# Kernel optimization log

Measured on AMD Instinct MI355X. Metric: run time of the kernel, lower is better.

The kernel has to match this reference:

```python
import jax, jax.numpy as jnp
import numpy as np

B, S, N = 4, 512, 2048
E = 1024          # expanded_size
QL, H, D, VL = 32, 8, 2, 32   # query_len, num_heads, num_duplicates, values_len
EPS = 1e-5


def setup_inputs() -> dict:
    key = jax.random.key(0)
    ks = jax.random.split(key, 8)
    return {
        "embeddings": jax.random.normal(ks[0], (B, S, E), jnp.float32),
        "keys": jax.random.normal(ks[1], (B, N, QL * H), jnp.float32),
        "values": jax.random.normal(ks[2], (B, N, VL * H), jnp.float32),
        "output_connectivity_sub": jax.random.normal(ks[3], (H, S * D, N), jnp.float32),
        "Wq": jax.random.normal(ks[4], (QL * H * D, E), jnp.float32) / np.sqrt(E),
        "bq": jnp.zeros((QL * H * D,), jnp.float32),
        "Wo": jax.random.normal(ks[5], (E, VL * H * D), jnp.float32) / np.sqrt(VL * H * D),
        "bo": jnp.zeros((E,), jnp.float32),
        "gamma": jnp.ones((VL * H * D,), jnp.float32),
        "beta": jnp.zeros((VL * H * D,), jnp.float32),
    }


def reference(embeddings, keys, values, output_connectivity_sub,
              Wq, bq, Wo, bo, gamma, beta):
    # query projection: [B,S,E] -> [B,S,QL*H*D]
    q = embeddings @ Wq.T + bq
    # view [B, S*D, QL*H] -> [B, S*D, QL, H] -> [B, H, S*D, QL]
    q = q.reshape(B, S * D, QL, H).transpose(0, 3, 1, 2)
    # keys: [B,N,QL*H] -> [B,N,QL,H] -> [B,H,QL,N]
    k = keys.reshape(B, N, QL, H).transpose(0, 3, 2, 1)
    # values: [B,N,VL*H] -> [B,N,VL,H] -> [B,H,N,VL]
    v = values.reshape(B, N, VL, H).transpose(0, 3, 1, 2)

    scores = jnp.einsum('bhsq,bhqn->bhsn', q, k) / np.sqrt(QL).astype(np.float32)
    probs = jax.nn.softmax(scores - output_connectivity_sub, axis=-1)
    vo = jnp.einsum('bhsn,bhnv->bhsv', probs, v)          # [B,H,S*D,VL]

    # [B,H,S*D,VL] -> [B,H,S,VL*D] -> [B,S,H,VL*D] -> [B,S,H*VL*D]
    vo = vo.reshape(B, H, S, VL * D).transpose(0, 2, 1, 3).reshape(B, S, H * VL * D)

    mean = jnp.mean(vo, axis=-1, keepdims=True)
    var = jnp.mean(jnp.square(vo - mean), axis=-1, keepdims=True)
    xn = (vo - mean) / jnp.sqrt(var + EPS) * gamma + beta
    return xn @ Wo.T + bo
```

## Files before the change

kernel.cpp:

```cpp
#include <hip/hip_runtime.h>
#include <hip/hip_bf16.h>


typedef short  short8 __attribute__((ext_vector_type(8)));
typedef float  f32x4  __attribute__((ext_vector_type(4)));

__device__ __forceinline__ ushort f2bf(float x) {
  union { float f; unsigned int u; } v; v.f = x;
  unsigned int r = v.u + 0x7fffu + ((v.u >> 16) & 1u);
  return (ushort)(r >> 16);
}

__device__ __forceinline__ unsigned int cvtpk(float a, float b) {
  unsigned int r;
  asm("v_cvt_pk_bf16_f32 %0, %1, %2" : "=v"(r) : "v"(a), "v"(b));
  return r;
}
__device__ __forceinline__ short8 cvt8(f32x4 a, f32x4 b) {
  union { unsigned int u[4]; short8 s; } r;
  r.u[0] = cvtpk(a[0], a[1]);
  r.u[1] = cvtpk(a[2], a[3]);
  r.u[2] = cvtpk(b[0], b[1]);
  r.u[3] = cvtpk(b[2], b[3]);
  return r.s;
}

#if __has_builtin(__builtin_amdgcn_global_load_lds)
#define OCS_ASYNC 1
__device__ __forceinline__ void gl_lds16(const float* g, float* l) {
  __builtin_amdgcn_global_load_lds(
      (const __attribute__((address_space(1))) unsigned int*)g,
      (__attribute__((address_space(3))) unsigned int*)l, 16, 0, 0);
}
#else
#define OCS_ASYNC 0
#endif

__device__ __forceinline__ void prep_body(
    char* smem, int bi,
    const float* __restrict__ keys, const float* __restrict__ values,
    ushort* __restrict__ kbf, ushort* __restrict__ vbf)
{
  ushort (*T)[264] = (ushort (*)[264])smem;
  const int b  = bi >> 6;
  const int n0 = (bi & 63) * 32;
  const int t  = threadIdx.x;
  const int nr = t >> 3;
  const int c0 = (t & 7) * 32;

  {
    const float* src = keys + ((size_t)b*2048 + n0 + nr)*256 + c0;
#pragma unroll
    for (int j = 0; j < 32; j += 8) {
      f32x4 x0 = *(const f32x4*)(src + j);
      f32x4 x1 = *(const f32x4*)(src + j + 4);
      *(short8*)&T[nr][c0 + j] = cvt8(x0, x1);
    }
  }
  __syncthreads();
  {
    const int h = t >> 5, nn = t & 31;
    const int pp = 16*((nn >> 2) & 1) + 4*(nn >> 3) + (nn & 3);
    ushort* dst = kbf + (((size_t)(b*8 + h) * 2048) + n0 + pp) * 32;
#pragma unroll
    for (int j = 0; j < 4; j++) {
      short8 w;
#pragma unroll
      for (int i = 0; i < 8; i++) w[i] = (short)T[nn][(j*8 + i)*8 + h];
      *(short8*)(dst + j*8) = w;
    }
  }
  __syncthreads();
  {
    const float* src = values + ((size_t)b*2048 + n0 + nr)*256 + c0;
#pragma unroll
    for (int j = 0; j < 32; j += 8) {
      f32x4 x0 = *(const f32x4*)(src + j);
      f32x4 x1 = *(const f32x4*)(src + j + 4);
      *(short8*)&T[nr][c0 + j] = cvt8(x0, x1);
    }
  }
  __syncthreads();
  {
    const int c = t, h = c & 7, vl = c >> 3;
    ushort* dst = vbf + (((size_t)(b*8 + h) * 32) + vl) * 2048 + n0;
#pragma unroll
    for (int j = 0; j < 4; j++) {
      short8 w;
#pragma unroll
      for (int i = 0; i < 8; i++) w[i] = (short)T[j*8 + i][c];
      *(short8*)(dst + j*8) = w;
    }
  }
}

template<int EPI>
__device__ __forceinline__ void gemm_body(
    char* smem,
    const float* __restrict__ A, const float* __restrict__ Bm,
    const float* __restrict__ bias, void* __restrict__ outp,
    int M, int N, int K, int m0, int n0,
    const float* __restrict__ rowsum, const float* __restrict__ rowsumsq,
    const float* __restrict__ gamma,  const float* __restrict__ beta)
{
  ushort* As = (ushort*)smem;
  ushort* Bs = (ushort*)(smem + 8192);
  const int tid = threadIdx.x;
  const int lane = tid & 63;
  const int wid  = tid >> 6;
  const int wm = wid >> 1, wn = wid & 1;
  const int lt = lane & 15, g = lane >> 4;
  const int lrow = tid >> 2;
  const int lseg = tid & 3;
  const int slot_w = lseg ^ ((lrow & 3) ^ ((lrow >> 2) & 3));

  f32x4 acc[2][2] = {};
  f32x4 pa0, pa1, pb0, pb1;

  float mean_r = 0.f, rstd_r = 1.f;
  if (EPI == 1) {
    const float s_  = rowsum[m0 + lrow];
    const float sq_ = rowsumsq[m0 + lrow];
    mean_r = s_ * (1.0f/512.0f);
    rstd_r = rsqrtf(sq_ * (1.0f/512.0f) - mean_r * mean_r + 1e-5f);
  }

#define GLOAD(K0) do {                                                        \
    const float* sa_ = A  + (size_t)(m0 + lrow) * K + (K0) + lseg * 8;        \
    pa0 = *(const f32x4*)sa_;  pa1 = *(const f32x4*)(sa_ + 4);                \
    const float* sb_ = Bm + (size_t)(n0 + lrow) * K + (K0) + lseg * 8;        \
    pb0 = *(const f32x4*)sb_;  pb1 = *(const f32x4*)(sb_ + 4);                \
  } while (0)
#define SWRITE(BUF, K0) do {                                                  \
    f32x4 qa0 = pa0, qa1 = pa1;                                               \
    if (EPI == 1) {                                                           \
      const float* gp_ = gamma + (K0) + lseg * 8;                             \
      const float* bp_ = beta  + (K0) + lseg * 8;                             \
      f32x4 g0_ = *(const f32x4*)gp_, g1_ = *(const f32x4*)(gp_ + 4);         \
      f32x4 b0_ = *(const f32x4*)bp_, b1_ = *(const f32x4*)(bp_ + 4);         \
      _Pragma("unroll")                                                       \
      for (int r_ = 0; r_ < 4; r_++) {                                        \
        qa0[r_] = (qa0[r_] - mean_r) * rstd_r * g0_[r_] + b0_[r_];            \
        qa1[r_] = (qa1[r_] - mean_r) * rstd_r * g1_[r_] + b1_[r_];            \
      }                                                                       \
    }                                                                         \
    *(short8*)&As[(BUF)*2048 + lrow*32 + slot_w * 8] = cvt8(qa0, qa1);        \
    *(short8*)&Bs[(BUF)*2048 + lrow*32 + slot_w * 8] = cvt8(pb0, pb1);        \
  } while (0)

  GLOAD(0);
  SWRITE(0, 0);
  __syncthreads();

  int cur = 0;
  for (int k0 = 0; k0 < K; k0 += 32) {
    const bool more = (k0 + 32 < K);
    if (more) GLOAD(k0 + 32);
    short8 af[2], bfr[2];
#pragma unroll
    for (int ss = 0; ss < 2; ss++) {
      const int ra = wm*32 + ss*16 + lt;
      af[ss]  = *(const short8*)&As[cur*2048 + ra*32 + (g ^ ((ra & 3) ^ ((ra >> 2) & 3))) * 8];
      const int rb = wn*32 + ss*16 + lt;
      bfr[ss] = *(const short8*)&Bs[cur*2048 + rb*32 + (g ^ ((rb & 3) ^ ((rb >> 2) & 3))) * 8];
    }
#pragma unroll
    for (int i = 0; i < 2; i++)
#pragma unroll
      for (int j = 0; j < 2; j++)
        acc[i][j] = __builtin_amdgcn_mfma_f32_16x16x32_bf16(af[i], bfr[j], acc[i][j], 0, 0, 0);
    asm volatile("s_barrier" ::: "memory");
    if (more) {
      SWRITE(cur ^ 1, k0 + 32);
      asm volatile("s_waitcnt lgkmcnt(0)" ::: "memory");
    }
    asm volatile("s_barrier" ::: "memory");
    cur ^= 1;
  }

#pragma unroll
  for (int i = 0; i < 2; i++)
#pragma unroll
    for (int j = 0; j < 2; j++) {
      const int n  = n0 + wn*32 + j*16 + lt;
      const float bv = bias[n];
      const int mb = m0 + wm*32 + i*16 + g*4;
#pragma unroll
      for (int r = 0; r < 4; r++) {
        const int mm = mb + r;
        if (EPI == 0) {
          const float val = (acc[i][j][r] + bv) * 0.17677669529663687f;
          const int bb = mm >> 9, s = mm & 511;
          const int d = n >> 8, ql = (n >> 3) & 31, hh = n & 7;
          const int tt = s*2 + d;
          ((ushort*)outp)[((size_t)(bb*8 + hh) * 1024 + tt) * 32 + ql] = f2bf(val);
        } else {
          ((float*)outp)[(size_t)mm * N + n] = acc[i][j][r] + bv;
        }
      }
    }
#undef GLOAD
#undef SWRITE
}

__global__ __launch_bounds__(256) void prep_gemm0(
    const float* __restrict__ keys, const float* __restrict__ values,
    ushort* __restrict__ kbf, ushort* __restrict__ vbf,
    const float* __restrict__ emb, const float* __restrict__ Wq,
    const float* __restrict__ bq, ushort* __restrict__ qbf)
{
  __shared__ __align__(16) char smem[17408];
  const int bi = blockIdx.x;
  if (bi < 256) {
    prep_body(smem, bi, keys, values, kbf, vbf);
  } else {
    const int gblk = bi - 256;
    const int m0 = (gblk & 31) * 64;
    const int n0 = (gblk >> 5) * 64;
    gemm_body<0>(smem, emb, Wq, bq, (void*)qbf, 2048, 512, 1024, m0, n0,
                 nullptr, nullptr, nullptr, nullptr);
  }
}

__global__ __launch_bounds__(256) void gemm1_ln(
    const float* __restrict__ vo, const float* __restrict__ Wo,
    const float* __restrict__ bo, float* __restrict__ outp,
    const float* __restrict__ rowsum, const float* __restrict__ rowsumsq,
    const float* __restrict__ gamma, const float* __restrict__ beta)
{
  __shared__ __align__(16) char smem[16384];
  gemm_body<1>(smem, vo, Wo, bo, (void*)outp, 2048, 1024, 512,
               blockIdx.x * 64, blockIdx.y * 64, rowsum, rowsumsq, gamma, beta);
}

__global__ __launch_bounds__(256) void attn_kernel(
    const ushort* __restrict__ qbf, const ushort* __restrict__ kbf,
    const ushort* __restrict__ vbf, const float* __restrict__ ocs,
    float* __restrict__ pacc, float* __restrict__ pl, int nsteps)
{
#if OCS_ASYNC
  __shared__ float obuf[4][2048];
#endif
  const int tid  = threadIdx.x;
  const int lane = tid & 63;
  const int id = blockIdx.x;
  const int h   = id & 7;
  const int ttp = (id >> 3) & 15;
  const int c   = id >> 7;
  const int b  = tid >> 6;
  const int wid0 = ((h << 5) + 2*ttp) * 4 + b;
  const int t0 = ttp * 64;
  const int lt = lane & 15, g = lane >> 4;
  const int n_start = c * nsteps * 32;

  const ushort* qp = qbf + (size_t)(b*8 + h) * (1024*32);
  const ushort* kp = kbf + (size_t)(b*8 + h) * (2048*32);
  const ushort* vp = vbf + (size_t)(b*8 + h) * (32*2048);
  const float*  op = ocs + (size_t)h * (1024*2048);

#define NSX(I) (((I) < nsteps) ? (n_start + (I)*32) : n_start)

  const int srow = tid >> 3;
  const int scol = 4 * ((tid & 7) ^ (srow & 7));
  const float* sb0 = op + (size_t)(t0 + srow) * 2048 + scol;
  const float* sb1 = op + (size_t)(t0 + 32 + srow) * 2048 + scol;
#if OCS_ASYNC
  const int ldsw = (tid & 192) * 16;
#define SL_ISSUE(STEP) do {                                                   \
    gl_lds16(sb0 + NSX(STEP), (float*)((char*)obuf + (((STEP) & 3) << 13) + ldsw));        \
    gl_lds16(sb1 + NSX(STEP), (float*)((char*)obuf + (((STEP) & 3) << 13) + 4096 + ldsw)); \
  } while (0)
  const int ro0 = lt * 128;
  const int ro1 = (16 + lt) * 128;
  const int c0x = ((2*g)     ^ (lt & 7)) * 16;
  const int c1x = ((2*g + 1) ^ (lt & 7)) * 16;
#define CO_READ(DST, TILE, STEP) do {                                         \
    const char* bb_ = (const char*)obuf + (((STEP) & 3) << 13) + ((TILE) << 12); \
    DST[0][0] = *(const f32x4*)(bb_ + ro0 + c0x);                             \
    DST[1][0] = *(const f32x4*)(bb_ + ro0 + c1x);                             \
    DST[0][1] = *(const f32x4*)(bb_ + ro1 + c0x);                             \
    DST[1][1] = *(const f32x4*)(bb_ + ro1 + c1x);                             \
  } while (0)
#define PAIR_SYNC() do {                                                      \
    __builtin_amdgcn_sched_barrier(0);                                        \
    asm volatile("s_waitcnt vmcnt(8)" ::: "memory");                          \
    __builtin_amdgcn_sched_barrier(0);                                        \
    __builtin_amdgcn_s_barrier();                                             \
  } while (0)
#else
#define SL_ISSUE(STEP)
#define CO_READ(DST, TILE, STEP) do {                                         \
    const int nn_ = NSX(STEP);                                                \
    const float* r0_ = op + (size_t)(t0 + (TILE)*32 + lt) * 2048 + nn_;       \
    const float* r1_ = op + (size_t)(t0 + (TILE)*32 + 16 + lt) * 2048 + nn_;  \
    DST[0][0] = *(const f32x4*)(r0_ + 8*g);                                   \
    DST[1][0] = *(const f32x4*)(r0_ + 8*g + 4);                               \
    DST[0][1] = *(const f32x4*)(r1_ + 8*g);                                   \
    DST[1][1] = *(const f32x4*)(r1_ + 8*g + 4);                               \
  } while (0)
#define PAIR_SYNC()
#endif

#define LD_KV(KD, VD, NN) do {                                                \
    KD[0] = *(const short8*)(kp + (size_t)((NN) + lt) * 32 + g*8);            \
    KD[1] = *(const short8*)(kp + (size_t)((NN) + 16 + lt) * 32 + g*8);       \
    VD[0] = *(const short8*)(vp + (size_t)lt * 2048 + (NN) + g*8);            \
    VD[1] = *(const short8*)(vp + (size_t)(16 + lt) * 2048 + (NN) + g*8);     \
  } while (0)

  short8 qf0[2], qf1[2];
#pragma unroll
  for (int ts = 0; ts < 2; ts++) {
    qf0[ts] = *(const short8*)(qp + (t0 + ts*16 + lt)*32 + g*8);
    qf1[ts] = *(const short8*)(qp + (t0 + 32 + ts*16 + lt)*32 + g*8);
  }

  f32x4 acc0[2][2] = {}, acc1[2][2] = {};
  float lsum0[2] = {0.f, 0.f}, lsum1[2] = {0.f, 0.f};
  const f32x4 fzero = {0.f, 0.f, 0.f, 0.f};

#define TSB(SC0, SC1, CO0, CO1, VLO, VHI, LS, ACCA, ACCB) do {                \
    float p0 = __expf(SC0[0] - CO0[0]);                                       \
    float p1 = __expf(SC0[1] - CO0[1]);                                       \
    float p2 = __expf(SC0[2] - CO0[2]);                                       \
    float p3 = __expf(SC0[3] - CO0[3]);                                       \
    float p4 = __expf(SC1[0] - CO1[0]);                                       \
    float p5 = __expf(SC1[1] - CO1[1]);                                       \
    float p6 = __expf(SC1[2] - CO1[2]);                                       \
    float p7 = __expf(SC1[3] - CO1[3]);                                       \
    LS += ((p0+p1)+(p2+p3)) + ((p4+p5)+(p6+p7));                              \
    union { unsigned int u[4]; short8 s; } pf;                                \
    pf.u[0] = (unsigned int)f2bf(p0) | ((unsigned int)f2bf(p1) << 16);        \
    pf.u[1] = (unsigned int)f2bf(p2) | ((unsigned int)f2bf(p3) << 16);        \
    pf.u[2] = (unsigned int)f2bf(p4) | ((unsigned int)f2bf(p5) << 16);        \
    pf.u[3] = (unsigned int)f2bf(p6) | ((unsigned int)f2bf(p7) << 16);        \
    ACCA = __builtin_amdgcn_mfma_f32_16x16x32_bf16(VLO, pf.s, ACCA, 0, 0, 0); \
    ACCB = __builtin_amdgcn_mfma_f32_16x16x32_bf16(VHI, pf.s, ACCB, 0, 0, 0); \
  } while (0)

#define STEPTILE(KC_, VC_, QFA, QFB, TILE, STEP, ACC, LS) do {                \
    f32x4 s0a = __builtin_amdgcn_mfma_f32_16x16x32_bf16(KC_[0], QFA, fzero, 0, 0, 0); \
    f32x4 s1a = __builtin_amdgcn_mfma_f32_16x16x32_bf16(KC_[1], QFA, fzero, 0, 0, 0); \
    f32x4 s0b = __builtin_amdgcn_mfma_f32_16x16x32_bf16(KC_[0], QFB, fzero, 0, 0, 0); \
    f32x4 s1b = __builtin_amdgcn_mfma_f32_16x16x32_bf16(KC_[1], QFB, fzero, 0, 0, 0); \
    f32x4 co[2][2];                                                           \
    CO_READ(co, TILE, STEP);                                                  \
    TSB(s0a, s1a, co[0][0], co[1][0], VC_[0], VC_[1], LS[0], ACC[0][0], ACC[0][1]); \
    TSB(s0b, s1b, co[0][1], co[1][1], VC_[0], VC_[1], LS[1], ACC[1][0], ACC[1][1]); \
  } while (0)

#define PAIR(SA_, KC, VC, KN, VN) do {                                        \
    const int sA_ = (SA_);                                                    \
    SL_ISSUE(sA_ + 2);                                                        \
    SL_ISSUE(sA_ + 3);                                                        \
    __builtin_amdgcn_sched_barrier(0);                                        \
    LD_KV(KN[0], VN[0], NSX(sA_ + 2));                                        \
    LD_KV(KN[1], VN[1], NSX(sA_ + 3));                                        \
    __builtin_amdgcn_sched_barrier(0);                                        \
    STEPTILE(KC[0], VC[0], qf0[0], qf0[1], 0, sA_,     acc0, lsum0);          \
    STEPTILE(KC[0], VC[0], qf1[0], qf1[1], 1, sA_,     acc1, lsum1);          \
    STEPTILE(KC[1], VC[1], qf0[0], qf0[1], 0, sA_ + 1, acc0, lsum0);          \
    STEPTILE(KC[1], VC[1], qf1[0], qf1[1], 1, sA_ + 1, acc1, lsum1);          \
    PAIR_SYNC();                                                              \
  } while (0)

  short8 KA[2][2], VA[2][2], KB[2][2], VB[2][2];

#if OCS_ASYNC
  SL_ISSUE(0); SL_ISSUE(1);
  __builtin_amdgcn_sched_barrier(0);
#endif
  LD_KV(KA[0], VA[0], NSX(0));
  LD_KV(KA[1], VA[1], NSX(1));
#if OCS_ASYNC
  __builtin_amdgcn_sched_barrier(0);
  asm volatile("s_waitcnt vmcnt(8)" ::: "memory");
  __builtin_amdgcn_s_barrier();
#endif

  for (int s = 0; s < nsteps; s += 4) {
    PAIR(s,     KA, VA, KB, VB);
    PAIR(s + 2, KB, VB, KA, VA);
  }
#undef PAIR
#undef STEPTILE
#undef TSB
#undef LD_KV
#undef CO_READ
#undef SL_ISSUE
#undef PAIR_SYNC
#undef NSX

  {
    float* pb0 = pacc + ((size_t)(c*1024 + wid0) * 4) * 256 + lane * 4;
    *(f32x4*)(pb0 + 0*256) = acc0[0][0];
    *(f32x4*)(pb0 + 1*256) = acc0[0][1];
    *(f32x4*)(pb0 + 2*256) = acc0[1][0];
    *(f32x4*)(pb0 + 3*256) = acc0[1][1];
    float* pb1 = pacc + ((size_t)(c*1024 + wid0 + 4) * 4) * 256 + lane * 4;
    *(f32x4*)(pb1 + 0*256) = acc1[0][0];
    *(f32x4*)(pb1 + 1*256) = acc1[0][1];
    *(f32x4*)(pb1 + 2*256) = acc1[1][0];
    *(f32x4*)(pb1 + 3*256) = acc1[1][1];
  }
#pragma unroll
  for (int ts = 0; ts < 2; ts++) {
    float L0 = lsum0[ts], L1 = lsum1[ts];
    L0 += __shfl_xor(L0, 16);  L0 += __shfl_xor(L0, 32);
    L1 += __shfl_xor(L1, 16);  L1 += __shfl_xor(L1, 32);
    if (g == 0) {
      pl[((size_t)(c*1024 + wid0)) * 32 + ts*16 + lt]     = L0;
      pl[((size_t)(c*1024 + wid0 + 4)) * 32 + ts*16 + lt] = L1;
    }
  }
}

__global__ __launch_bounds__(256) void combine_kernel(
    const float* __restrict__ pacc, const float* __restrict__ pl,
    float* __restrict__ vo, float* __restrict__ rowsum,
    float* __restrict__ rowsumsq, int NS)
{
  const int lane = threadIdx.x & 63;
  const int wid = blockIdx.x * 4 + (threadIdx.x >> 6);
  const int b  = wid & 3;
  const int tt = (wid >> 2) & 31;
  const int h  = wid >> 7;
  const int t0 = tt * 32;
  const int lt = lane & 15, g = lane >> 4;

  f32x4 acc[4] = {};
  float L[2] = {0.f, 0.f};
  for (int cc = 0; cc < NS; ++cc) {
    const float* pb = pacc + ((size_t)(cc*1024 + wid) * 4) * 256 + lane * 4;
#pragma unroll
    for (int q = 0; q < 4; q++) {
      f32x4 v = *(const f32x4*)(pb + q * 256);
#pragma unroll
      for (int r = 0; r < 4; r++) acc[q][r] += v[r];
    }
    L[0] += pl[((size_t)(cc*1024 + wid)) * 32 + lt];
    L[1] += pl[((size_t)(cc*1024 + wid)) * 32 + 16 + lt];
  }
#pragma unroll
  for (int ts = 0; ts < 2; ts++) {
    const float inv = 1.0f / L[ts];
    const int t = t0 + ts*16 + lt;
    const int s = t >> 1, d = t & 1;
    const int row = b*512 + s;
    float* dst = vo + ((size_t)row * 512) + h*64 + d*32;
    float psum = 0.f, psq = 0.f;
#pragma unroll
    for (int vs = 0; vs < 2; vs++) {
      f32x4 o;
#pragma unroll
      for (int r = 0; r < 4; r++) {
        o[r] = acc[ts*2 + vs][r] * inv;
        psum += o[r];
        psq  += o[r] * o[r];
      }
      *(f32x4*)(dst + vs*16 + g*4) = o;
    }
    psum += __shfl_xor(psum, 16);  psum += __shfl_xor(psum, 32);
    psq  += __shfl_xor(psq, 16);   psq  += __shfl_xor(psq, 32);
    if (g == 0) {
      atomicAdd(&rowsum[row], psum);
      atomicAdd(&rowsumsq[row], psq);
    }
  }
}

extern "C" void kernel_launch(void* const* d_in, const int* in_sizes, int n_in,
                              void* d_out, int out_size, void* d_ws, size_t ws_size,
                              hipStream_t stream)
{
  const float* emb    = (const float*)d_in[0];
  const float* keys   = (const float*)d_in[1];
  const float* values = (const float*)d_in[2];
  const float* ocs    = (const float*)d_in[3];
  const float* Wq     = (const float*)d_in[4];
  const float* bq     = (const float*)d_in[5];
  const float* Wo     = (const float*)d_in[6];
  const float* bo     = (const float*)d_in[7];
  const float* gamma  = (const float*)d_in[8];
  const float* beta   = (const float*)d_in[9];

  char* ws = (char*)d_ws;
  ushort* qbf = (ushort*)(ws);
  ushort* kbf = (ushort*)(ws + (2u << 20));
  ushort* vbf = (ushort*)(ws + (6u << 20));
  float*  vo  = (float*) (ws + (10u << 20));
  const size_t pbase = (size_t)14u << 20;

  int NS;
  if      (ws_size >= ((size_t)48u << 20)) NS = 8;
  else if (ws_size >= ((size_t)31u << 20)) NS = 4;
  else if (ws_size >= ((size_t)23u << 20)) NS = 2;
  else                                     NS = 1;
  float* pacc = (float*)(ws + pbase);
  float* pl   = (float*)(ws + pbase + (size_t)NS * (4u << 20));
  float* rsum = (float*)(ws + pbase + (size_t)NS * (4u << 20) + (size_t)NS * (128u << 10));
  float* rsq  = rsum + 2048;
  const int nsteps = 2048 / (NS * 32);

  prep_gemm0<<<dim3(512), dim3(256), 0, stream>>>(keys, values, kbf, vbf,
                                                  emb, Wq, bq, qbf);
  attn_kernel<<<dim3(128 * NS), dim3(256), 0, stream>>>(qbf, kbf, vbf, ocs, pacc, pl, nsteps);
  hipMemsetAsync(rsum, 0, 2 * 2048 * sizeof(float), stream);
  combine_kernel<<<dim3(256), dim3(256), 0, stream>>>(pacc, pl, vo, rsum, rsq, NS);
  gemm1_ln<<<dim3(32, 16), dim3(256), 0, stream>>>(vo, Wo, bo, (float*)d_out,
                                                   rsum, rsq, gamma, beta);
}
```

Before: 86.79 us.

## Template attention on step count, fold stats memset into prep, cap split at four

Makes the attention step count a template parameter so the main loop fully unrolls and the step bounds become constants. Adds s_setprio around the MFMA compute section so a wave keeps issue priority while it computes. Removes the separate hipMemsetAsync by having four extra blocks in the prep kernel zero the row-statistics buffer. Also caps the key-split factor at 4 instead of 8, which changes grid size and occupancy for large workspaces. Full unrolling raises code size and register pressure.

```diff
diff --git a/kernel.cpp b/kernel.cpp
--- a/kernel.cpp
+++ b/kernel.cpp
@@ -207,18 +207,24 @@
     const float* __restrict__ keys, const float* __restrict__ values,
     ushort* __restrict__ kbf, ushort* __restrict__ vbf,
     const float* __restrict__ emb, const float* __restrict__ Wq,
-    const float* __restrict__ bq, ushort* __restrict__ qbf)
+    const float* __restrict__ bq, ushort* __restrict__ qbf,
+    float* __restrict__ stats)
 {
   __shared__ __align__(16) char smem[17408];
   const int bi = blockIdx.x;
   if (bi < 256) {
     prep_body(smem, bi, keys, values, kbf, vbf);
-  } else {
+  } else if (bi < 512) {
     const int gblk = bi - 256;
     const int m0 = (gblk & 31) * 64;
     const int n0 = (gblk >> 5) * 64;
     gemm_body<0>(smem, emb, Wq, bq, (void*)qbf, 2048, 512, 1024, m0, n0,
                  nullptr, nullptr, nullptr, nullptr);
+  } else {
+    stats[(bi - 512) * 1024 + threadIdx.x * 4 + 0] = 0.f;
+    stats[(bi - 512) * 1024 + threadIdx.x * 4 + 1] = 0.f;
+    stats[(bi - 512) * 1024 + threadIdx.x * 4 + 2] = 0.f;
+    stats[(bi - 512) * 1024 + threadIdx.x * 4 + 3] = 0.f;
   }
 }
 
@@ -233,10 +239,11 @@
                blockIdx.x * 64, blockIdx.y * 64, rowsum, rowsumsq, gamma, beta);
 }
 
+template<int NSTEPS>
 __global__ __launch_bounds__(256) void attn_kernel(
     const ushort* __restrict__ qbf, const ushort* __restrict__ kbf,
     const ushort* __restrict__ vbf, const float* __restrict__ ocs,
-    float* __restrict__ pacc, float* __restrict__ pl, int nsteps)
+    float* __restrict__ pacc, float* __restrict__ pl)
 {
 #if OCS_ASYNC
   __shared__ float obuf[4][2048];
@@ -251,14 +258,14 @@
   const int wid0 = ((h << 5) + 2*ttp) * 4 + b;
   const int t0 = ttp * 64;
   const int lt = lane & 15, g = lane >> 4;
-  const int n_start = c * nsteps * 32;
+  const int n_start = c * NSTEPS * 32;
 
   const ushort* qp = qbf + (size_t)(b*8 + h) * (1024*32);
   const ushort* kp = kbf + (size_t)(b*8 + h) * (2048*32);
   const ushort* vp = vbf + (size_t)(b*8 + h) * (32*2048);
   const float*  op = ocs + (size_t)h * (1024*2048);
 
-#define NSX(I) (((I) < nsteps) ? (n_start + (I)*32) : n_start)
+#define NSX(I) (((I) < NSTEPS) ? (n_start + (I)*32) : n_start)
 
   const int srow = tid >> 3;
   const int scol = 4 * ((tid & 7) ^ (srow & 7));
@@ -357,10 +364,12 @@
     LD_KV(KN[0], VN[0], NSX(sA_ + 2));                                        \
     LD_KV(KN[1], VN[1], NSX(sA_ + 3));                                        \
     __builtin_amdgcn_sched_barrier(0);                                        \
+    __builtin_amdgcn_s_setprio(1);                                            \
     STEPTILE(KC[0], VC[0], qf0[0], qf0[1], 0, sA_,     acc0, lsum0);          \
     STEPTILE(KC[0], VC[0], qf1[0], qf1[1], 1, sA_,     acc1, lsum1);          \
     STEPTILE(KC[1], VC[1], qf0[0], qf0[1], 0, sA_ + 1, acc0, lsum0);          \
     STEPTILE(KC[1], VC[1], qf1[0], qf1[1], 1, sA_ + 1, acc1, lsum1);          \
+    __builtin_amdgcn_s_setprio(0);                                            \
     PAIR_SYNC();                                                              \
   } while (0)
 
@@ -378,7 +387,8 @@
   __builtin_amdgcn_s_barrier();
 #endif
 
-  for (int s = 0; s < nsteps; s += 4) {
+#pragma unroll
+  for (int s = 0; s < NSTEPS; s += 4) {
     PAIR(s,     KA, VA, KB, VB);
     PAIR(s + 2, KB, VB, KA, VA);
   }
@@ -492,20 +502,22 @@
   const size_t pbase = (size_t)14u << 20;
 
   int NS;
-  if      (ws_size >= ((size_t)48u << 20)) NS = 8;
-  else if (ws_size >= ((size_t)31u << 20)) NS = 4;
+  if      (ws_size >= ((size_t)31u << 20)) NS = 4;
   else if (ws_size >= ((size_t)23u << 20)) NS = 2;
   else                                     NS = 1;
   float* pacc = (float*)(ws + pbase);
   float* pl   = (float*)(ws + pbase + (size_t)NS * (4u << 20));
   float* rsum = (float*)(ws + pbase + (size_t)NS * (4u << 20) + (size_t)NS * (128u << 10));
   float* rsq  = rsum + 2048;
-  const int nsteps = 2048 / (NS * 32);
-
-  prep_gemm0<<<dim3(512), dim3(256), 0, stream>>>(keys, values, kbf, vbf,
-                                                  emb, Wq, bq, qbf);
-  attn_kernel<<<dim3(128 * NS), dim3(256), 0, stream>>>(qbf, kbf, vbf, ocs, pacc, pl, nsteps);
-  hipMemsetAsync(rsum, 0, 2 * 2048 * sizeof(float), stream);
+
+  prep_gemm0<<<dim3(516), dim3(256), 0, stream>>>(keys, values, kbf, vbf,
+                                                  emb, Wq, bq, qbf, rsum);
+  if (NS == 4)
+    attn_kernel<16><<<dim3(512), dim3(256), 0, stream>>>(qbf, kbf, vbf, ocs, pacc, pl);
+  else if (NS == 2)
+    attn_kernel<32><<<dim3(256), dim3(256), 0, stream>>>(qbf, kbf, vbf, ocs, pacc, pl);
+  else
+    attn_kernel<64><<<dim3(128), dim3(256), 0, stream>>>(qbf, kbf, vbf, ocs, pacc, pl);
   combine_kernel<<<dim3(256), dim3(256), 0, stream>>>(pacc, pl, vo, rsum, rsq, NS);
   gemm1_ln<<<dim3(32, 16), dim3(256), 0, stream>>>(vo, Wo, bo, (float*)d_out,
                                                    rsum, rsq, gamma, beta);
```

Result: no change. 87.98 us (+1.4%).
